# Kernel optimization log

Measured on AMD Instinct MI355X. Metric: run time of the kernel, lower is better.

The kernel has to match this reference:

```python
import jax, jax.numpy as jnp
import numpy as np

C_Z = 128
C_H = 128
N = 512
B = 1

def _layer_norm(x, g, b, eps=1e-5):
    mu = jnp.mean(x, axis=-1, keepdims=True)
    var = jnp.var(x, axis=-1, keepdims=True)
    return (x - mu) * jax.lax.rsqrt(var + eps) * g + b

def _linear(x, w, b):
    # torch Linear: y = x @ w.T + b, w: [out, in]
    return jnp.einsum('...i,oi->...o', x, w) + b

def setup_inputs() -> dict:
    key = jax.random.key(0)
    ks = jax.random.split(key, 8)
    s = 1.0 / np.sqrt(C_Z)
    return {
        'z': jax.random.normal(ks[0], (B, N, N, C_Z), jnp.float32),
        'mask': jnp.ones((B, N, N), jnp.float32),
        'ln_in_g': jnp.ones((C_Z,), jnp.float32),
        'ln_in_b': jnp.zeros((C_Z,), jnp.float32),
        'w_ag': jax.random.normal(ks[1], (C_H, C_Z), jnp.float32) * s,
        'b_ag': jnp.ones((C_H,), jnp.float32),
        'w_ap': jax.random.normal(ks[2], (C_H, C_Z), jnp.float32) * s,
        'b_ap': jnp.zeros((C_H,), jnp.float32),
        'w_bg': jax.random.normal(ks[3], (C_H, C_Z), jnp.float32) * s,
        'b_bg': jnp.ones((C_H,), jnp.float32),
        'w_bp': jax.random.normal(ks[4], (C_H, C_Z), jnp.float32) * s,
        'b_bp': jnp.zeros((C_H,), jnp.float32),
        'w_g': jax.random.normal(ks[5], (C_Z, C_Z), jnp.float32) * s,
        'b_g': jnp.zeros((C_Z,), jnp.float32),
        'w_z': jax.random.normal(ks[6], (C_Z, C_H), jnp.float32) * s,
        'b_z': jnp.zeros((C_Z,), jnp.float32),
        'ln_out_g': jnp.ones((C_H,), jnp.float32),
        'ln_out_b': jnp.zeros((C_H,), jnp.float32),
    }

def reference(z, mask, ln_in_g, ln_in_b, w_ag, b_ag, w_ap, b_ap,
              w_bg, b_bg, w_bp, b_bp, w_g, b_g, w_z, b_z,
              ln_out_g, ln_out_b):
    m = mask[..., None]                       # [B,N,N,1]
    zn = _layer_norm(z, ln_in_g, ln_in_b)     # [B,N,N,Cz]
    a = m * jax.nn.sigmoid(_linear(zn, w_ag, b_ag)) * _linear(zn, w_ap, b_ap)
    b = m * jax.nn.sigmoid(_linear(zn, w_bg, b_bg)) * _linear(zn, w_bp, b_bp)
    # outgoing: x[b,i,j,c] = sum_k a[b,i,k,c] * b[b,j,k,c]
    x = jnp.einsum('bikc,bjkc->bijc', a, b)
    x = _layer_norm(x, ln_out_g, ln_out_b)
    x = _linear(x, w_z, b_z)
    g = jax.nn.sigmoid(_linear(zn, w_g, b_g))
    return x * g
```

## Files before the change

### kernel.cpp

```cpp
#include <hip/hip_runtime.h>

#define NN 512
#define CCH 128
#define MM (NN*NN)

using f32x4  = __attribute__((ext_vector_type(4))) float;
using f32x2  = __attribute__((ext_vector_type(2))) float;
using bf16x8 = __attribute__((ext_vector_type(8))) short;
using u16x4  = __attribute__((ext_vector_type(4))) unsigned short;
using u32x2  = __attribute__((ext_vector_type(2))) unsigned int;
using u32x4  = __attribute__((ext_vector_type(4))) unsigned int;
typedef unsigned short u16;

__device__ __forceinline__ u16 f2bf(float f) {
    unsigned u = __builtin_bit_cast(unsigned, f);
    u += 0x7FFF + ((u >> 16) & 1);
    return (u16)(u >> 16);
}
__device__ __forceinline__ float bf2f(u16 h) {
    unsigned u = ((unsigned)h) << 16;
    return __builtin_bit_cast(float, u);
}
__device__ __forceinline__ unsigned pack2(float lo, float hi) {
    return (unsigned)f2bf(lo) | ((unsigned)f2bf(hi) << 16);
}
__device__ __forceinline__ float sigm(float x) { return 1.0f / (1.0f + __expf(-x)); }

__device__ __forceinline__ void gl_lds16(const void* g, void* l) {
    __builtin_amdgcn_global_load_lds(
        (const __attribute__((address_space(1))) void*)g,
        (__attribute__((address_space(3))) void*)l, 16, 0, 0);
}

__global__ __launch_bounds__(256) void k_prep(
    const float* __restrict__ w0, const float* __restrict__ w1,
    const float* __restrict__ w2, const float* __restrict__ w3,
    const float* __restrict__ w4, const float* __restrict__ w5,
    const float* __restrict__ b0, const float* __restrict__ b1,
    const float* __restrict__ b2, const float* __restrict__ b3,
    const float* __restrict__ b4, const float* __restrict__ b5,
    const float* __restrict__ gin, const float* __restrict__ bin,
    const float* __restrict__ gout, const float* __restrict__ bout,
    u16* __restrict__ wbf, float* __restrict__ bias2) {
    int mat = blockIdx.x;
    const float* W = mat==0?w0:mat==1?w1:mat==2?w2:mat==3?w3:mat==4?w4:w5;
    const float* B = mat==0?b0:mat==1?b1:mat==2?b2:mat==3?b3:mat==4?b4:b5;
    const float* G = (mat==5)? gout : gin;
    const float* Bt= (mat==5)? bout : bin;
    __shared__ float gs[CCH], bs[CCH];
    int tid = threadIdx.x;
    if (tid < CCH) { gs[tid] = G[tid]; bs[tid] = Bt[tid]; }
    __syncthreads();
    int o = tid >> 1, c0 = (tid & 1) * 64;
    const float* src = W + o * CCH + c0;
    char* dstrow = (char*)(wbf + mat * 16384) + o * 256;
    int key = o & 7;
    float dot = 0.f;
    #pragma unroll
    for (int q = 0; q < 16; ++q) {
        f32x4 v = *(const f32x4*)(src + q * 4);
        int c = c0 + q * 4;
        dot += bs[c]*v.x + bs[c+1]*v.y + bs[c+2]*v.z + bs[c+3]*v.w;
        u16x4 p;
        p.x = f2bf(v.x * gs[c]);     p.y = f2bf(v.y * gs[c+1]);
        p.z = f2bf(v.z * gs[c+2]);   p.w = f2bf(v.w * gs[c+3]);
        int chunk = (c0 >> 3) + (q >> 1);
        *(u16x4*)(dstrow + (((chunk ^ key)) << 4) + ((q & 1) << 3)) = p;
    }
    dot += __shfl_xor(dot, 1);
    if ((tid & 1) == 0) bias2[mat * CCH + o] = B[o] + dot;
}

__global__ __launch_bounds__(256) void k_ln(const float* __restrict__ z,
                                            u16* __restrict__ zn) {
    int tid = threadIdx.x;
    int w = tid >> 6, lane = tid & 63;
    long row = (long)blockIdx.x * 4 + w;
    f32x2 v = *(const f32x2*)(z + row * CCH + lane * 2);
    float s = v.x + v.y, s2 = v.x * v.x + v.y * v.y;
    #pragma unroll
    for (int off = 32; off; off >>= 1) {
        s  += __shfl_xor(s, off);
        s2 += __shfl_xor(s2, off);
    }
    float mu  = s * (1.0f / CCH);
    float var = fmaxf(s2 * (1.0f / CCH) - mu * mu, 0.f);
    float rs  = rsqrtf(var + 1e-5f);
    unsigned pk = pack2((v.x - mu) * rs, (v.y - mu) * rs);
    *(unsigned*)(zn + row * CCH + lane * 2) = pk;
}

__global__ __launch_bounds__(256) void k_proj(
    const u16* __restrict__ zn, const float* __restrict__ mask,
    const u16* __restrict__ wbf, const float* __restrict__ bias2,
    u16* __restrict__ aT, u16* __restrict__ bT, u16* gateB) {
    __shared__ __align__(16) u16 w1s[16384];
    __shared__ __align__(16) u16 w2s[16384];
    int tid = threadIdx.x, w = tid >> 6, lane = tid & 63;
    int r = lane & 15, kq = lane >> 4;
    int mode = blockIdx.y;
    int mat1 = (mode == 2) ? 4 : mode * 2;
    long m0 = (long)blockIdx.x * 64;

    const char* W1g = (const char*)(wbf + mat1 * 16384);
    const char* W2g = (const char*)(wbf + (mat1 + 1) * 16384);
    #pragma unroll
    for (int it = 0; it < 8; ++it) {
        long off = (long)it * 4096 + tid * 16;
        gl_lds16(W1g + off, (char*)w1s + it * 4096 + w * 1024);
        if (mode < 2) gl_lds16(W2g + off, (char*)w2s + it * 4096 + w * 1024);
    }

    bf16x8 av[4];
    long mrow = m0 + w * 16 + r;
    #pragma unroll
    for (int kb = 0; kb < 4; ++kb)
        av[kb] = *(const bf16x8*)(zn + mrow * CCH + kb * 32 + kq * 8);

    f32x4 mkv = {1.f, 1.f, 1.f, 1.f};
    if (mode < 2) mkv = *(const f32x4*)(mask + m0 + w * 16 + kq * 4);

    __syncthreads();

    if (mode < 2) {
        u16* dst = mode ? bT : aT;
        const float* B1 = bias2 + mat1 * CCH;
        const float* B2 = bias2 + (mat1 + 1) * CCH;
        int i7 = (int)((blockIdx.x >> 3) & 7);

        f32x4 acc1[8], acc2[8];
        #pragma unroll
        for (int nt = 0; nt < 8; ++nt) { acc1[nt] = {0,0,0,0}; acc2[nt] = {0,0,0,0}; }
        #pragma unroll
        for (int nt = 0; nt < 8; ++nt) {
            int ol = nt * 16 + r;
            int key = ol & 7;
            const char* row1 = (const char*)w1s + ol * 256;
            const char* row2 = (const char*)w2s + ol * 256;
            #pragma unroll
            for (int kb = 0; kb < 4; ++kb) {
                int ph = ((kb * 4 + kq) ^ key) << 4;
                bf16x8 b1 = *(const bf16x8*)(row1 + ph);
                bf16x8 b2 = *(const bf16x8*)(row2 + ph);
                acc1[nt] = __builtin_amdgcn_mfma_f32_16x16x32_bf16(av[kb], b1, acc1[nt], 0, 0, 0);
                acc2[nt] = __builtin_amdgcn_mfma_f32_16x16x32_bf16(av[kb], b2, acc2[nt], 0, 0, 0);
            }
        }
        __syncthreads();
        char* tb = (char*)w1s;
        int moff2 = (w * 16 + kq * 4) * 2;
        #pragma unroll
        for (int nt = 0; nt < 8; ++nt) {
            int cc = nt * 16 + r;
            float b1v = B1[cc], b2v = B2[cc];
            float v0 = mkv[0] * sigm(acc1[nt][0] + b1v) * (acc2[nt][0] + b2v);
            float v1 = mkv[1] * sigm(acc1[nt][1] + b1v) * (acc2[nt][1] + b2v);
            float v2 = mkv[2] * sigm(acc1[nt][2] + b1v) * (acc2[nt][2] + b2v);
            float v3 = mkv[3] * sigm(acc1[nt][3] + b1v) * (acc2[nt][3] + b2v);
            u32x2 pv; pv.x = pack2(v0, v1); pv.y = pack2(v2, v3);
            *(u32x2*)(tb + cc * 144 + moff2) = pv;
        }
        __syncthreads();
        int q = tid & 7;
        long gbase = m0 * 2 + ((long)(q ^ i7) << 4);
        #pragma unroll
        for (int rd = 0; rd < 4; ++rd) {
            int cc = rd * 32 + (tid >> 3);
            u32x4 vv = *(const u32x4*)(tb + cc * 144 + q * 16);
            *(u32x4*)((char*)dst + ((long)cc << 19) + gbase) = vv;
        }
    } else {
        f32x4 acc[8];
        #pragma unroll
        for (int nt = 0; nt < 8; ++nt) acc[nt] = {0,0,0,0};
        #pragma unroll
        for (int nt = 0; nt < 8; ++nt) {
            int ol = nt * 16 + r;
            int key = ol & 7;
            const char* row1 = (const char*)w1s + ol * 256;
            #pragma unroll
            for (int kb = 0; kb < 4; ++kb) {
                bf16x8 b1 = *(const bf16x8*)(row1 + (((kb * 4 + kq) ^ key) << 4));
                acc[nt] = __builtin_amdgcn_mfma_f32_16x16x32_bf16(b1, av[kb], acc[nt], 0, 0, 0);
            }
        }
        long m = m0 + w * 16 + r;
        #pragma unroll
        for (int nt = 0; nt < 8; ++nt) {
            int c0 = nt * 16 + kq * 4;
            f32x4 bg = *(const f32x4*)(bias2 + 4 * CCH + c0);
            u32x2 pv;
            pv.x = pack2(sigm(acc[nt][0] + bg[0]), sigm(acc[nt][1] + bg[1]));
            pv.y = pack2(sigm(acc[nt][2] + bg[2]), sigm(acc[nt][3] + bg[3]));
            *(u32x2*)(gateB + m * 256 + c0) = pv;
        }
    }
}

__global__ __launch_bounds__(256, 4) void k_tri(const u16* __restrict__ aT,
                                                const u16* __restrict__ bT,
                                                u16* __restrict__ xT) {
    __shared__ __align__(16) char shm[34816];
    u16* At = (u16*)shm;
    u16* Bt = (u16*)(shm + 16384);
    int tid = threadIdx.x;
    int w = tid >> 6, lane = tid & 63;
    int r = lane & 15, kq = lane >> 4;

    int L = blockIdx.x;
    int xcd = L & 7, idx = L >> 3;
    int c    = xcd + 8 * (idx >> 4);
    int tile = idx & 15;
    int ti = tile >> 2, tj = tile & 3;

    const char* abase = (const char*)(aT + (long)c * MM) + (long)(ti * 128) * 1024;
    const char* bbase = (const char*)(bT + (long)c * MM) + (long)(tj * 128) * 1024;
    int wm = w >> 1, wn = w & 1;

    f32x4 acc[4][4];
    #pragma unroll
    for (int a = 0; a < 4; ++a)
        #pragma unroll
        for (int bq = 0; bq < 4; ++bq) acc[a][bq] = {0.f,0.f,0.f,0.f};

    for (int ks = 0; ks < 8; ++ks) {
        const char* asrc = abase + ks * 128;
        const char* bsrc = bbase + ks * 128;
        #pragma unroll
        for (int it = 0; it < 4; ++it) {
            int u = it * 256 + tid;
            long goff = (long)(u >> 3) * 1024 + (u & 7) * 16;
            gl_lds16(asrc + goff, (char*)At + it * 4096 + w * 1024);
            gl_lds16(bsrc + goff, (char*)Bt + it * 4096 + w * 1024);
        }
        __syncthreads();

        #pragma unroll
        for (int kh = 0; kh < 2; ++kh) {
            bf16x8 af[4];
            #pragma unroll
            for (int mt = 0; mt < 4; ++mt) {
                int rowa = wm * 64 + mt * 16 + r;
                af[mt] = *(const bf16x8*)((const char*)At + rowa * 128 +
                                          (((kh * 4 + kq) ^ (r & 7)) << 4));
            }
            #pragma unroll
            for (int nt = 0; nt < 4; ++nt) {
                int rowb = wn * 64 + nt * 16 + r;
                bf16x8 bf = *(const bf16x8*)((const char*)Bt + rowb * 128 +
                                             (((kh * 4 + kq) ^ (r & 7)) << 4));
                #pragma unroll
                for (int mt = 0; mt < 4; ++mt)
                    acc[mt][nt] = __builtin_amdgcn_mfma_f32_16x16x32_bf16(bf, af[mt], acc[mt][nt], 0, 0, 0);
            }
        }
        __syncthreads();
    }

    char* tb = shm;
    #pragma unroll
    for (int mt = 0; mt < 4; ++mt) {
        int il = wm * 64 + mt * 16 + r;
        #pragma unroll
        for (int nt = 0; nt < 4; ++nt) {
            int jl = wn * 64 + nt * 16 + kq * 4;
            u32x2 pv;
            pv.x = pack2(acc[mt][nt][0], acc[mt][nt][1]);
            pv.y = pack2(acc[mt][nt][2], acc[mt][nt][3]);
            *(u32x2*)(tb + il * 272 + jl * 2) = pv;
        }
    }
    __syncthreads();
    u16* xrow = xT + (long)c * MM + (long)(ti * 128) * NN + tj * 128;
    int joff = tid & 15;
    #pragma unroll
    for (int rd = 0; rd < 8; ++rd) {
        int il = rd * 16 + (tid >> 4);
        u32x4 vv = *(const u32x4*)(tb + il * 272 + joff * 16);
        *(u32x4*)(xrow + (long)il * NN + joff * 8) = vv;
    }
}

__global__ __launch_bounds__(256, 4) void k_out(const u16* __restrict__ xT,
                                                const u16* __restrict__ wbf,
                                                const float* __restrict__ bias2,
                                                const u16* gateB,
                                                float* __restrict__ outp) {
    __shared__ __align__(16) u16 xl[64 * 128];
    int tid = threadIdx.x, w = tid >> 6, lane = tid & 63;
    int r = lane & 15, kq = lane >> 4;
    long m0 = (long)blockIdx.x * 64;

    {
        int cg = tid & 31, ms = tid >> 5;
        int c0 = cg * 4;
        const u16* base = xT + m0 + (long)ms * 8;
        bf16x8 v0 = *(const bf16x8*)(base + (long)(c0 + 0) * MM);
        bf16x8 v1 = *(const bf16x8*)(base + (long)(c0 + 1) * MM);
        bf16x8 v2 = *(const bf16x8*)(base + (long)(c0 + 2) * MM);
        bf16x8 v3 = *(const bf16x8*)(base + (long)(c0 + 3) * MM);
        #pragma unroll
        for (int e = 0; e < 8; ++e) {
            int m = ms * 8 + e;
            u16x4 t;
            t.x = (u16)v0[e]; t.y = (u16)v1[e]; t.z = (u16)v2[e]; t.w = (u16)v3[e];
            *(u16x4*)((char*)xl + m * 256 + ((c0 * 2) ^ ((m & 15) << 4))) = t;
        }
    }
    __syncthreads();

    int mlr = w * 16 + r;
    int swm = (mlr & 15) << 4;
    u32x4 avu[4];
    float s = 0.f, s2 = 0.f;
    #pragma unroll
    for (int kb = 0; kb < 4; ++kb) {
        avu[kb] = *(const u32x4*)((const char*)xl + mlr * 256 + ((kb * 64 + kq * 16) ^ swm));
        #pragma unroll
        for (int p = 0; p < 4; ++p) {
            unsigned u = avu[kb][p];
            float flo = __builtin_bit_cast(float, u << 16);
            float fhi = __builtin_bit_cast(float, u & 0xFFFF0000u);
            s += flo + fhi;
            s2 = fmaf(flo, flo, s2);
            s2 = fmaf(fhi, fhi, s2);
        }
    }
    s  += __shfl_xor(s, 16);  s  += __shfl_xor(s, 32);
    s2 += __shfl_xor(s2, 16); s2 += __shfl_xor(s2, 32);
    float mu = s * (1.0f / CCH);
    float var = fmaxf(s2 * (1.0f / CCH) - mu * mu, 0.f);
    float rs = rsqrtf(var + 1e-5f);
    float nmu = -mu * rs;
    bf16x8 av[4];
    #pragma unroll
    for (int kb = 0; kb < 4; ++kb) {
        u32x4 o;
        #pragma unroll
        for (int p = 0; p < 4; ++p) {
            unsigned u = avu[kb][p];
            float flo = __builtin_bit_cast(float, u << 16);
            float fhi = __builtin_bit_cast(float, u & 0xFFFF0000u);
            o[p] = pack2(fmaf(flo, rs, nmu), fmaf(fhi, rs, nmu));
        }
        av[kb] = __builtin_bit_cast(bf16x8, o);
    }

    long m = m0 + w * 16 + r;
    u16x4 gvu[8];
    #pragma unroll
    for (int nt = 0; nt < 8; ++nt)
        gvu[nt] = *(const u16x4*)(gateB + m * 256 + nt * 16 + kq * 4);

    const char* Wz = (const char*)(wbf + 5 * 16384);
    f32x4 acc[8];
    #pragma unroll
    for (int nt = 0; nt < 8; ++nt) acc[nt] = {0,0,0,0};
    #pragma unroll
    for (int nt = 0; nt < 8; ++nt) {
        int ol = nt * 16 + r;
        int key = ol & 7;
        const char* row = Wz + ol * 256;
        #pragma unroll
        for (int kb = 0; kb < 4; ++kb) {
            bf16x8 bw = *(const bf16x8*)(row + (((kb * 4 + kq) ^ key) << 4));
            acc[nt] = __builtin_amdgcn_mfma_f32_16x16x32_bf16(bw, av[kb], acc[nt], 0, 0, 0);
        }
    }

    __syncthreads();

    const float* b2z = bias2 + 5 * CCH;
    #pragma unroll
    for (int nt = 0; nt < 8; ++nt) {
        int c0 = nt * 16 + kq * 4;
        f32x4 bb = *(const f32x4*)(b2z + c0);
        f32x4 o;
        #pragma unroll
        for (int j = 0; j < 4; ++j)
            o[j] = (acc[nt][j] + bb[j]) * bf2f(gvu[nt][j]);
        *(f32x4*)(outp + m * CCH + c0) = o;
    }
}

extern "C" void kernel_launch(void* const* d_in, const int* in_sizes, int n_in,
                              void* d_out, int out_size, void* d_ws, size_t ws_size,
                              hipStream_t stream) {
    const float* z       = (const float*)d_in[0];
    const float* mask    = (const float*)d_in[1];
    const float* ln_in_g = (const float*)d_in[2];
    const float* ln_in_b = (const float*)d_in[3];
    const float* w_ag    = (const float*)d_in[4];
    const float* b_ag    = (const float*)d_in[5];
    const float* w_ap    = (const float*)d_in[6];
    const float* b_ap    = (const float*)d_in[7];
    const float* w_bg    = (const float*)d_in[8];
    const float* b_bg    = (const float*)d_in[9];
    const float* w_bp    = (const float*)d_in[10];
    const float* b_bp    = (const float*)d_in[11];
    const float* w_g     = (const float*)d_in[12];
    const float* b_g     = (const float*)d_in[13];
    const float* w_z     = (const float*)d_in[14];
    const float* b_z     = (const float*)d_in[15];
    const float* ln_o_g  = (const float*)d_in[16];
    const float* ln_o_b  = (const float*)d_in[17];
    float* out = (float*)d_out;
    u16* gateB = (u16*)d_out;

    char* ws = (char*)d_ws;
    const size_t SL = (size_t)MM * CCH * 2;
    u16* xT   = (u16*)ws;
    u16* aT   = (u16*)(ws + SL);
    u16* bT   = (u16*)(ws + 2 * SL);
    u16* zn   = (u16*)(ws + 3 * SL);
    u16* wbf  = (u16*)(ws + 4 * SL);
    float* b2 = (float*)(ws + 4 * SL + 6 * 16384 * 2);

    k_prep<<<6, 256, 0, stream>>>(w_ag, w_ap, w_bg, w_bp, w_g, w_z,
                                  b_ag, b_ap, b_bg, b_bp, b_g, b_z,
                                  ln_in_g, ln_in_b, ln_o_g, ln_o_b, wbf, b2);
    k_ln<<<MM / 4, 256, 0, stream>>>(z, zn);
    k_proj<<<dim3(MM / 64, 3), 256, 0, stream>>>(zn, mask, wbf, b2, aT, bT, gateB);
    k_tri<<<2048, 256, 0, stream>>>(aT, bT, xT);
    k_out<<<MM / 64, 256, 0, stream>>>(xT, wbf, b2, gateB, out);
}
```

Baseline: 332.4 us.

## Fuse input layernorm into projection kernel and compute all projections per block

Merges k_ln and the three-mode k_proj into a single kernel. Each block normalizes its 64 rows of z into swizzled shared memory, then reloads weights into LDS in phases to compute the a, b and gate projections. This removes the bf16 zn round trip through global memory and the repeated reads of zn across three grid modes. The transposed a/b stores now go straight to global memory without LDS staging, which may give less coalesced writes, and the serial weight reloads add synchronisation inside each block.

```diff
diff --git a/kernel.cpp b/kernel.cpp
--- a/kernel.cpp
+++ b/kernel.cpp
@@ -71,63 +71,81 @@
     if ((tid & 1) == 0) bias2[mat * CCH + o] = B[o] + dot;
 }
 
-__global__ __launch_bounds__(256) void k_ln(const float* __restrict__ z,
-                                            u16* __restrict__ zn) {
-    int tid = threadIdx.x;
-    int w = tid >> 6, lane = tid & 63;
-    long row = (long)blockIdx.x * 4 + w;
-    f32x2 v = *(const f32x2*)(z + row * CCH + lane * 2);
-    float s = v.x + v.y, s2 = v.x * v.x + v.y * v.y;
-    #pragma unroll
-    for (int off = 32; off; off >>= 1) {
-        s  += __shfl_xor(s, off);
-        s2 += __shfl_xor(s2, off);
-    }
-    float mu  = s * (1.0f / CCH);
-    float var = fmaxf(s2 * (1.0f / CCH) - mu * mu, 0.f);
-    float rs  = rsqrtf(var + 1e-5f);
-    unsigned pk = pack2((v.x - mu) * rs, (v.y - mu) * rs);
-    *(unsigned*)(zn + row * CCH + lane * 2) = pk;
-}
-
-__global__ __launch_bounds__(256) void k_proj(
-    const u16* __restrict__ zn, const float* __restrict__ mask,
+__global__ __launch_bounds__(256) void k_fused(
+    const float* __restrict__ z, const float* __restrict__ mask,
     const u16* __restrict__ wbf, const float* __restrict__ bias2,
     u16* __restrict__ aT, u16* __restrict__ bT, u16* gateB) {
-    __shared__ __align__(16) u16 w1s[16384];
-    __shared__ __align__(16) u16 w2s[16384];
+    __shared__ __align__(16) u16 znt[8192];
+    __shared__ __align__(16) u16 wls[32768];
     int tid = threadIdx.x, w = tid >> 6, lane = tid & 63;
     int r = lane & 15, kq = lane >> 4;
-    int mode = blockIdx.y;
-    int mat1 = (mode == 2) ? 4 : mode * 2;
     long m0 = (long)blockIdx.x * 64;
 
-    const char* W1g = (const char*)(wbf + mat1 * 16384);
-    const char* W2g = (const char*)(wbf + (mat1 + 1) * 16384);
-    #pragma unroll
-    for (int it = 0; it < 8; ++it) {
-        long off = (long)it * 4096 + tid * 16;
-        gl_lds16(W1g + off, (char*)w1s + it * 4096 + w * 1024);
-        if (mode < 2) gl_lds16(W2g + off, (char*)w2s + it * 4096 + w * 1024);
-    }
+    {
+        const char* Wg = (const char*)wbf;
+        #pragma unroll
+        for (int it = 0; it < 16; ++it)
+            gl_lds16(Wg + (long)it * 4096 + tid * 16, (char*)wls + it * 4096 + w * 1024);
+    }
+
+    {
+        int row = tid >> 2, p = tid & 3, c0 = p * 32;
+        const float* zr = z + (m0 + row) * CCH + c0;
+        f32x4 va[8];
+        float s = 0.f, s2 = 0.f;
+        #pragma unroll
+        for (int q = 0; q < 8; ++q) {
+            va[q] = *(const f32x4*)(zr + q * 4);
+            s  += va[q].x + va[q].y + va[q].z + va[q].w;
+            s2 += va[q].x*va[q].x + va[q].y*va[q].y + va[q].z*va[q].z + va[q].w*va[q].w;
+        }
+        s += __shfl_xor(s, 1);  s += __shfl_xor(s, 2);
+        s2 += __shfl_xor(s2, 1); s2 += __shfl_xor(s2, 2);
+        float mu = s * (1.0f / CCH);
+        float var = fmaxf(s2 * (1.0f / CCH) - mu * mu, 0.f);
+        float rs = rsqrtf(var + 1e-5f);
+        int sw = (row & 15) << 4;
+        #pragma unroll
+        for (int q2 = 0; q2 < 4; ++q2) {
+            f32x4 v0 = va[q2*2], v1 = va[q2*2+1];
+            u32x2 pk;
+            pk.x = pack2((v0.x-mu)*rs, (v0.y-mu)*rs);
+            pk.y = pack2((v0.z-mu)*rs, (v0.w-mu)*rs);
+            u32x2 pk2;
+            pk2.x = pack2((v1.x-mu)*rs, (v1.y-mu)*rs);
+            pk2.y = pack2((v1.z-mu)*rs, (v1.w-mu)*rs);
+            char* p8 = (char*)znt + row * 256 + ((c0 * 2 + q2 * 16) ^ sw);
+            *(u32x2*)p8 = pk;
+            *(u32x2*)(p8 + 8) = pk2;
+        }
+    }
+    __syncthreads();
 
     bf16x8 av[4];
-    long mrow = m0 + w * 16 + r;
-    #pragma unroll
-    for (int kb = 0; kb < 4; ++kb)
-        av[kb] = *(const bf16x8*)(zn + mrow * CCH + kb * 32 + kq * 8);
-
-    f32x4 mkv = {1.f, 1.f, 1.f, 1.f};
-    if (mode < 2) mkv = *(const f32x4*)(mask + m0 + w * 16 + kq * 4);
-
-    __syncthreads();
-
-    if (mode < 2) {
-        u16* dst = mode ? bT : aT;
-        const float* B1 = bias2 + mat1 * CCH;
-        const float* B2 = bias2 + (mat1 + 1) * CCH;
-        int i7 = (int)((blockIdx.x >> 3) & 7);
-
+    {
+        int row = w * 16 + r, sw = (row & 15) << 4;
+        #pragma unroll
+        for (int kb = 0; kb < 4; ++kb)
+            av[kb] = *(const bf16x8*)((const char*)znt + row * 256 + ((kb * 64 + kq * 16) ^ sw));
+    }
+    f32x4 mkv = *(const f32x4*)(mask + m0 + w * 16 + kq * 4);
+
+    int i7 = (int)((blockIdx.x >> 3) & 7);
+    int qch = w * 2 + (kq >> 1);
+    long boff = m0 * 2 + (long)((qch ^ i7) << 4) + ((kq & 1) << 3);
+
+    #pragma unroll 1
+    for (int ph = 0; ph < 2; ++ph) {
+        if (ph == 1) {
+            __syncthreads();
+            const char* Wg = (const char*)wbf + 65536;
+            #pragma unroll
+            for (int it = 0; it < 16; ++it)
+                gl_lds16(Wg + (long)it * 4096 + tid * 16, (char*)wls + it * 4096 + w * 1024);
+            __syncthreads();
+        }
+        const float* B1 = bias2 + (ph * 2) * CCH;
+        const float* B2 = bias2 + (ph * 2 + 1) * CCH;
         f32x4 acc1[8], acc2[8];
         #pragma unroll
         for (int nt = 0; nt < 8; ++nt) { acc1[nt] = {0,0,0,0}; acc2[nt] = {0,0,0,0}; }
@@ -135,20 +153,18 @@
         for (int nt = 0; nt < 8; ++nt) {
             int ol = nt * 16 + r;
             int key = ol & 7;
-            const char* row1 = (const char*)w1s + ol * 256;
-            const char* row2 = (const char*)w2s + ol * 256;
+            const char* row1 = (const char*)wls + ol * 256;
+            const char* row2 = (const char*)wls + 32768 + ol * 256;
             #pragma unroll
             for (int kb = 0; kb < 4; ++kb) {
-                int ph = ((kb * 4 + kq) ^ key) << 4;
-                bf16x8 b1 = *(const bf16x8*)(row1 + ph);
-                bf16x8 b2 = *(const bf16x8*)(row2 + ph);
+                int ph16 = ((kb * 4 + kq) ^ key) << 4;
+                bf16x8 b1 = *(const bf16x8*)(row1 + ph16);
+                bf16x8 b2 = *(const bf16x8*)(row2 + ph16);
                 acc1[nt] = __builtin_amdgcn_mfma_f32_16x16x32_bf16(av[kb], b1, acc1[nt], 0, 0, 0);
                 acc2[nt] = __builtin_amdgcn_mfma_f32_16x16x32_bf16(av[kb], b2, acc2[nt], 0, 0, 0);
             }
         }
-        __syncthreads();
-        char* tb = (char*)w1s;
-        int moff2 = (w * 16 + kq * 4) * 2;
+        u16* dst = ph ? bT : aT;
         #pragma unroll
         for (int nt = 0; nt < 8; ++nt) {
             int cc = nt * 16 + r;
@@ -158,18 +174,19 @@
             float v2 = mkv[2] * sigm(acc1[nt][2] + b1v) * (acc2[nt][2] + b2v);
             float v3 = mkv[3] * sigm(acc1[nt][3] + b1v) * (acc2[nt][3] + b2v);
             u32x2 pv; pv.x = pack2(v0, v1); pv.y = pack2(v2, v3);
-            *(u32x2*)(tb + cc * 144 + moff2) = pv;
-        }
-        __syncthreads();
-        int q = tid & 7;
-        long gbase = m0 * 2 + ((long)(q ^ i7) << 4);
-        #pragma unroll
-        for (int rd = 0; rd < 4; ++rd) {
-            int cc = rd * 32 + (tid >> 3);
-            u32x4 vv = *(const u32x4*)(tb + cc * 144 + q * 16);
-            *(u32x4*)((char*)dst + ((long)cc << 19) + gbase) = vv;
-        }
-    } else {
+            *(u32x2*)((char*)dst + ((long)cc << 19) + boff) = pv;
+        }
+    }
+
+    __syncthreads();
+    {
+        const char* Wg = (const char*)wbf + 131072;
+        #pragma unroll
+        for (int it = 0; it < 8; ++it)
+            gl_lds16(Wg + (long)it * 4096 + tid * 16, (char*)wls + it * 4096 + w * 1024);
+    }
+    __syncthreads();
+    {
         f32x4 acc[8];
         #pragma unroll
         for (int nt = 0; nt < 8; ++nt) acc[nt] = {0,0,0,0};
@@ -177,7 +194,7 @@
         for (int nt = 0; nt < 8; ++nt) {
             int ol = nt * 16 + r;
             int key = ol & 7;
-            const char* row1 = (const char*)w1s + ol * 256;
+            const char* row1 = (const char*)wls + ol * 256;
             #pragma unroll
             for (int kb = 0; kb < 4; ++kb) {
                 bf16x8 b1 = *(const bf16x8*)(row1 + (((kb * 4 + kq) ^ key) << 4));
@@ -412,15 +429,13 @@
     u16* xT   = (u16*)ws;
     u16* aT   = (u16*)(ws + SL);
     u16* bT   = (u16*)(ws + 2 * SL);
-    u16* zn   = (u16*)(ws + 3 * SL);
-    u16* wbf  = (u16*)(ws + 4 * SL);
-    float* b2 = (float*)(ws + 4 * SL + 6 * 16384 * 2);
+    u16* wbf  = (u16*)(ws + 3 * SL);
+    float* b2 = (float*)(ws + 3 * SL + 6 * 16384 * 2);
 
     k_prep<<<6, 256, 0, stream>>>(w_ag, w_ap, w_bg, w_bp, w_g, w_z,
                                   b_ag, b_ap, b_bg, b_bp, b_g, b_z,
                                   ln_in_g, ln_in_b, ln_o_g, ln_o_b, wbf, b2);
-    k_ln<<<MM / 4, 256, 0, stream>>>(z, zn);
-    k_proj<<<dim3(MM / 64, 3), 256, 0, stream>>>(zn, mask, wbf, b2, aT, bT, gateB);
+    k_fused<<<MM / 64, 256, 0, stream>>>(z, mask, wbf, b2, aT, bT, gateB);
     k_tri<<<2048, 256, 0, stream>>>(aT, bT, xT);
     k_out<<<MM / 64, 256, 0, stream>>>(xT, wbf, b2, gateB, out);
 }
```

New measurement: 316.8 us. 1.05x faster.
